# Optimization experiments

Hardware: AMD Instinct MI355X
Metric: run time of the kernel (lower is better)

The kernel has to match this reference:

```python
import jax, jax.numpy as jnp
import numpy as np

STATE_DIM = 5
HIDDEN = 32
B, S = 128, 4096
D_IN = STATE_DIM + 1 + 3  # [h_prev, temp_seq, direction]


def setup_inputs() -> dict:
    key = jax.random.key(0)
    ks = jax.random.split(key, 16)
    g = lambda k, shp: (jax.random.normal(k, shp, dtype=jnp.float32) * 0.1)
    z = lambda shp: jnp.zeros(shp, jnp.float32)
    inp = {}
    inp["h_prev"] = jax.random.normal(ks[0], (B, S, STATE_DIM), dtype=jnp.float32)
    inp["delta_x"] = jax.random.uniform(ks[1], (B, S, 6), dtype=jnp.float32)
    # internal layer 0 (input D_IN -> HIDDEN), layer 1 (HIDDEN -> HIDDEN)
    inp["Wa0"] = g(ks[2], (D_IN, HIDDEN)); inp["ba0"] = z((HIDDEN,))
    inp["Wb0"] = g(ks[3], (D_IN, HIDDEN)); inp["bb0"] = z((HIDDEN,))
    inp["Wa1"] = g(ks[4], (HIDDEN, HIDDEN)); inp["ba1"] = z((HIDDEN,))
    inp["Wb1"] = g(ks[5], (HIDDEN, HIDDEN)); inp["bb1"] = z((HIDDEN,))
    inp["W_alpha"] = g(ks[6], (HIDDEN, 1)); inp["b_alpha"] = z((1,))
    inp["W_beta"]  = g(ks[7], (HIDDEN, 1)); inp["b_beta"]  = z((1,))
    inp["W_gamma"] = g(ks[8], (HIDDEN, 1)); inp["b_gamma"] = z((1,))
    inp["W_c"] = g(ks[9], (HIDDEN, STATE_DIM)); inp["b_c"] = z((STATE_DIM,))
    inp["W_out"] = g(ks[10], (STATE_DIM, 1))  # no bias
    return inp


def reference(h_prev, delta_x, Wa0, ba0, Wb0, bb0, Wa1, ba1, Wb1, bb1,
              W_alpha, b_alpha, W_beta, b_beta, W_gamma, b_gamma,
              W_c, b_c, W_out):
    # delta_x: [delta_strain, delta_time, delta_temp, init_strain, init_time, init_temp]
    df = delta_x[..., :3]                       # (B, S, 3)
    init_temp = delta_x[:, 0:1, 5:6]            # (B, 1, 1) init temp at t=0
    temp_seq = jnp.cumsum(delta_x[..., 2:3], axis=1) + init_temp  # (B, S, 1)
    # normalized increment direction
    norm = jnp.maximum(jnp.sqrt(jnp.sum(df * df, axis=-1, keepdims=True)), 1e-7)
    direction = df / norm                       # (B, S, 3)
    l = jnp.concatenate([h_prev, temp_seq, direction], axis=-1)   # (B, S, 9)
    # two internal tanh*tanh gated dense layers
    l = jnp.tanh(l @ Wa0 + ba0) * jnp.tanh(l @ Wb0 + bb0)         # (B, S, 32)
    l = jnp.tanh(l @ Wa1 + ba1) * jnp.tanh(l @ Wb1 + bb1)         # (B, S, 32)
    # exp gates (non-negative rate params)
    alpha = jnp.exp(l @ W_alpha + b_alpha)      # (B, S, 1)
    beta  = jnp.exp(l @ W_beta  + b_beta)
    gamma = jnp.exp(l @ W_gamma + b_gamma)
    c_n = jnp.tanh(l @ W_c + b_c)               # (B, S, 5)
    # update gate from physical increments
    z = 1.0 - jnp.exp(-alpha * jnp.abs(df[..., 0:1])
                      - beta * df[..., 1:2]
                      - gamma * jnp.abs(df[..., 2:3]))
    h_n = (1.0 - z) * h_prev + z * c_n          # (B, S, 5)
    sigma_n = h_n @ W_out                       # (B, S, 1)
    return (h_n, sigma_n)
```

## Files before the change

kernel.cpp:

```cpp
#include <hip/hip_runtime.h>

#define B_DIMC   128
#define S_DIMC   4096
#define N_TOK    (B_DIMC * S_DIMC)
#define CHUNK    256
#define N_CHUNK  (N_TOK / CHUNK)
#define CPB      (S_DIMC / CHUNK)

typedef __attribute__((ext_vector_type(8))) short  short8;
typedef __attribute__((ext_vector_type(4))) float  floatx4;
typedef __attribute__((ext_vector_type(4))) int    intx4;

__device__ float g_chunksums[N_CHUNK];

__device__ __forceinline__ unsigned short f2bf(float f) {
    unsigned u = __builtin_bit_cast(unsigned, f);
    u = (u + 0x7FFFu + ((u >> 16) & 1u)) >> 16;
    return (unsigned short)u;
}
__device__ __forceinline__ int packbf(float a, float b) {
    return (int)f2bf(a) | ((int)f2bf(b) << 16);
}
__device__ __forceinline__ float fast_tanh(float x) {
    float xc = fminf(fmaxf(x, -9.0f), 9.0f);
    float e  = __builtin_amdgcn_exp2f(2.885390082f * xc);
    return fmaf(-2.0f, __builtin_amdgcn_rcpf(e + 1.0f), 1.0f);
}

__global__ __launch_bounds__(256) void chunksum_kernel(const float* __restrict__ dx) {
    const int t    = blockIdx.x * CHUNK + threadIdx.x;
    const int lane = threadIdx.x & 63;
    const int wid  = threadIdx.x >> 6;
    __shared__ float wsum[4];
    float x = dx[(size_t)t * 6 + 2];
    #pragma unroll
    for (int off = 32; off >= 1; off >>= 1) x += __shfl_down(x, off, 64);
    if (lane == 0) wsum[wid] = x;
    __syncthreads();
    if (threadIdx.x == 0)
        g_chunksums[blockIdx.x] = wsum[0] + wsum[1] + wsum[2] + wsum[3];
}

__device__ __forceinline__ float head_w(int n, int k,
                                        const float* Wal, const float* Wbe,
                                        const float* Wga, const float* Wc) {
    if (n == 0) return Wal[k];
    if (n == 1) return Wbe[k];
    if (n == 2) return Wga[k];
    if (n < 8)  return Wc[k * 5 + (n - 3)];
    return 0.0f;
}

__global__ __launch_bounds__(256) void msc_kernel(
    const float* __restrict__ h_prev, const float* __restrict__ dx,
    const float* __restrict__ Wa0, const float* __restrict__ ba0,
    const float* __restrict__ Wb0, const float* __restrict__ bb0,
    const float* __restrict__ Wa1, const float* __restrict__ ba1,
    const float* __restrict__ Wb1, const float* __restrict__ bb1,
    const float* __restrict__ W_alpha, const float* __restrict__ b_alpha,
    const float* __restrict__ W_beta,  const float* __restrict__ b_beta,
    const float* __restrict__ W_gamma, const float* __restrict__ b_gamma,
    const float* __restrict__ W_c,     const float* __restrict__ b_c,
    const float* __restrict__ W_out,
    float* __restrict__ out)
{
    __shared__ __align__(16) short sW[4][32][40];
    __shared__ __align__(16) short sWh[16][40];
    __shared__ __align__(16) short sA[4][64][40];
    __shared__ __align__(16) float sTemps[4][64];
    __shared__ float sBias[16];
    __shared__ float sWsum[4];

    const int tid  = threadIdx.x;
    const int w    = tid >> 6;
    const int lane = tid & 63;
    const int n    = lane & 15;
    const int quad = lane >> 4;
    const int t    = blockIdx.x * CHUNK + tid;

    const float* hp = h_prev + (size_t)t * 5;
    const float* d  = dx     + (size_t)t * 6;
    const float hp0 = hp[0], hp1 = hp[1], hp2 = hp[2], hp3 = hp[3], hp4 = hp[4];
    const float df0 = d[0], df1 = d[1], df2 = d[2];

    const int batch = blockIdx.x / CPB;
    const int cib   = blockIdx.x % CPB;
    float coff = dx[(size_t)batch * S_DIMC * 6 + 5];
    #pragma unroll
    for (int c = 0; c < CPB - 1; ++c)
        if (c < cib) coff += g_chunksums[batch * CPB + c];

    float w5a[2], w5b[2], bA0[2], bB0[2], bA1[2], bB1[2];
    #pragma unroll
    for (int nt = 0; nt < 2; ++nt) {
        const int col = nt * 16 + n;
        w5a[nt] = Wa0[5 * 32 + col];  w5b[nt] = Wb0[5 * 32 + col];
        bA0[nt] = ba0[col];           bB0[nt] = bb0[col];
        bA1[nt] = ba1[col];           bB1[nt] = bb1[col];
    }

    float x = df2;
    #pragma unroll
    for (int off = 1; off < 64; off <<= 1) {
        float y = __shfl_up(x, off, 64);
        if (lane >= off) x += y;
    }
    if (lane == 63) sWsum[w] = x;

    const float nrm = fmaxf(sqrtf(df0*df0 + df1*df1 + df2*df2), 1e-7f);
    const float inv = __builtin_amdgcn_rcpf(nrm);
    {
        int* arow = (int*)&sA[w][lane][0];
        intx4 v0 = { packbf(hp0, hp1), packbf(hp2, hp3),
                     packbf(hp4, 0.0f), packbf(df0*inv, df1*inv) };
        intx4 v1 = { packbf(df2*inv, 0.0f), 0, 0, 0 };
        intx4 z  = { 0, 0, 0, 0 };
        *(intx4*)&arow[0]  = v0;
        *(intx4*)&arow[4]  = v1;
        *(intx4*)&arow[8]  = z;
        *(intx4*)&arow[12] = z;
    }

    #pragma unroll
    for (int m = 0; m < 4; ++m) {
        const float* Wsrc = (m == 0) ? Wa0 : (m == 1) ? Wb0 : (m == 2) ? Wa1 : Wb1;
        const bool l0 = (m < 2);
        #pragma unroll
        for (int dd = tid; dd < 512; dd += 256) {
            const int col = dd >> 4, kd = dd & 15, k0 = kd * 2, k1 = k0 + 1;
            float v0, v1;
            if (l0) {
                v0 = (k0 < 9 && k0 != 5) ? Wsrc[k0 * 32 + col] : 0.0f;
                v1 = (k1 < 9 && k1 != 5) ? Wsrc[k1 * 32 + col] : 0.0f;
            } else {
                v0 = Wsrc[k0 * 32 + col];
                v1 = Wsrc[k1 * 32 + col];
            }
            ((int*)&sW[m][col][0])[kd] = packbf(v0, v1);
        }
    }
    {
        const int hn = tid >> 4, kd = tid & 15, k0 = kd * 2;
        const float v0 = head_w(hn, k0,     W_alpha, W_beta, W_gamma, W_c);
        const float v1 = head_w(hn, k0 + 1, W_alpha, W_beta, W_gamma, W_c);
        ((int*)&sWh[hn][0])[kd] = packbf(v0, v1);
    }
    if (tid < 16) {
        sBias[tid] = (tid == 0) ? b_alpha[0] : (tid == 1) ? b_beta[0]
                   : (tid == 2) ? b_gamma[0] : (tid < 8) ? b_c[tid - 3] : 0.0f;
    }

    __syncthreads();

    float pre = coff;
    if (w > 0) pre += sWsum[0];
    if (w > 1) pre += sWsum[1];
    if (w > 2) pre += sWsum[2];
    const float temp_t = pre + x;
    sTemps[w][lane] = temp_t;

    short8 Ba0f[2], Bb0f[2], Ba1f[2], Bb1f[2], Bhf;
    #pragma unroll
    for (int nt = 0; nt < 2; ++nt) {
        const int col = nt * 16 + n;
        Ba0f[nt] = *(const short8*)&sW[0][col][quad * 8];
        Bb0f[nt] = *(const short8*)&sW[1][col][quad * 8];
        Ba1f[nt] = *(const short8*)&sW[2][col][quad * 8];
        Bb1f[nt] = *(const short8*)&sW[3][col][quad * 8];
    }
    Bhf = *(const short8*)&sWh[n][quad * 8];
    const float hbias = sBias[n];

    #pragma unroll
    for (int mt = 0; mt < 4; ++mt) {
        const short8  Af = *(const short8*)&sA[w][mt * 16 + n][quad * 8];
        const floatx4 tv = *(const floatx4*)&sTemps[w][mt * 16 + quad * 4];
        #pragma unroll
        for (int nt = 0; nt < 2; ++nt) {
            floatx4 Ca, Cb;
            #pragma unroll
            for (int r = 0; r < 4; ++r) {
                Ca[r] = fmaf(tv[r], w5a[nt], bA0[nt]);
                Cb[r] = fmaf(tv[r], w5b[nt], bB0[nt]);
            }
            Ca = __builtin_amdgcn_mfma_f32_16x16x32_bf16(Af, Ba0f[nt], Ca, 0, 0, 0);
            Cb = __builtin_amdgcn_mfma_f32_16x16x32_bf16(Af, Bb0f[nt], Cb, 0, 0, 0);
            #pragma unroll
            for (int r = 0; r < 4; ++r) {
                const float gv = fast_tanh(Ca[r]) * fast_tanh(Cb[r]);
                sA[w][mt * 16 + quad * 4 + r][nt * 16 + n] = (short)f2bf(gv);
            }
        }
    }

    #pragma unroll
    for (int mt = 0; mt < 4; ++mt) {
        const short8 Af = *(const short8*)&sA[w][mt * 16 + n][quad * 8];
        #pragma unroll
        for (int nt = 0; nt < 2; ++nt) {
            floatx4 Ca = { bA1[nt], bA1[nt], bA1[nt], bA1[nt] };
            floatx4 Cb = { bB1[nt], bB1[nt], bB1[nt], bB1[nt] };
            Ca = __builtin_amdgcn_mfma_f32_16x16x32_bf16(Af, Ba1f[nt], Ca, 0, 0, 0);
            Cb = __builtin_amdgcn_mfma_f32_16x16x32_bf16(Af, Bb1f[nt], Cb, 0, 0, 0);
            #pragma unroll
            for (int r = 0; r < 4; ++r) {
                const float gv = fast_tanh(Ca[r]) * fast_tanh(Cb[r]);
                sA[w][mt * 16 + quad * 4 + r][nt * 16 + n] = (short)f2bf(gv);
            }
        }
    }

    short8 Ah[4];
    #pragma unroll
    for (int mt = 0; mt < 4; ++mt)
        Ah[mt] = *(const short8*)&sA[w][mt * 16 + n][quad * 8];
    __syncthreads();

    float* hc = (float*)&sA[w][0][0];
    #pragma unroll
    for (int mt = 0; mt < 4; ++mt) {
        floatx4 C = { hbias, hbias, hbias, hbias };
        C = __builtin_amdgcn_mfma_f32_16x16x32_bf16(Ah[mt], Bhf, C, 0, 0, 0);
        if (n < 8) {
            #pragma unroll
            for (int r = 0; r < 4; ++r)
                hc[(mt * 16 + quad * 4 + r) * 12 + n] = C[r];
        }
    }

    const floatx4 h0v = *(const floatx4*)&hc[lane * 12];
    const floatx4 h1v = *(const floatx4*)&hc[lane * 12 + 4];

    const float alpha = __expf(h0v[0]);
    const float beta  = __expf(h0v[1]);
    const float gamma = __expf(h0v[2]);
    const float z     = 1.0f - __expf(-(alpha * fabsf(df0) + beta * df1 + gamma * fabsf(df2)));
    const float omz   = 1.0f - z;

    const float c0 = fast_tanh(h0v[3]), c1 = fast_tanh(h1v[0]), c2 = fast_tanh(h1v[1]),
                c3 = fast_tanh(h1v[2]), c4 = fast_tanh(h1v[3]);

    const float hn0 = omz * hp0 + z * c0;
    const float hn1 = omz * hp1 + z * c1;
    const float hn2 = omz * hp2 + z * c2;
    const float hn3 = omz * hp3 + z * c3;
    const float hn4 = omz * hp4 + z * c4;

    float* out_h = out + (size_t)t * 5;
    out_h[0] = hn0; out_h[1] = hn1; out_h[2] = hn2; out_h[3] = hn3; out_h[4] = hn4;
    out[(size_t)N_TOK * 5 + t] =
        hn0 * W_out[0] + hn1 * W_out[1] + hn2 * W_out[2] + hn3 * W_out[3] + hn4 * W_out[4];
}

extern "C" void kernel_launch(void* const* d_in, const int* in_sizes, int n_in,
                              void* d_out, int out_size, void* d_ws, size_t ws_size,
                              hipStream_t stream) {
    const float* h_prev  = (const float*)d_in[0];
    const float* dx      = (const float*)d_in[1];
    const float* Wa0     = (const float*)d_in[2];
    const float* ba0     = (const float*)d_in[3];
    const float* Wb0     = (const float*)d_in[4];
    const float* bb0     = (const float*)d_in[5];
    const float* Wa1     = (const float*)d_in[6];
    const float* ba1     = (const float*)d_in[7];
    const float* Wb1     = (const float*)d_in[8];
    const float* bb1     = (const float*)d_in[9];
    const float* W_alpha = (const float*)d_in[10];
    const float* b_alpha = (const float*)d_in[11];
    const float* W_beta  = (const float*)d_in[12];
    const float* b_beta  = (const float*)d_in[13];
    const float* W_gamma = (const float*)d_in[14];
    const float* b_gamma = (const float*)d_in[15];
    const float* W_c     = (const float*)d_in[16];
    const float* b_c     = (const float*)d_in[17];
    const float* W_out   = (const float*)d_in[18];
    float* out = (float*)d_out;

    chunksum_kernel<<<N_CHUNK, CHUNK, 0, stream>>>(dx);
    msc_kernel<<<N_CHUNK, CHUNK, 0, stream>>>(
        h_prev, dx,
        Wa0, ba0, Wb0, bb0, Wa1, ba1, Wb1, bb1,
        W_alpha, b_alpha, W_beta, b_beta, W_gamma, b_gamma,
        W_c, b_c, W_out, out);
}
```

Measured before the change: 137.3 us.

## Load MFMA weight fragments directly to registers and fuse tanh-gate product

Weight B-fragments are now built per lane straight from global memory into registers, removing the shared-memory weight staging and its bias array. The chunk-prefix offset becomes a lane-parallel xor-shuffle reduction instead of a serial loop. The tanh*tanh gate is merged algebraically into one reciprocal and uses fmed3 clamping, and launch bounds request 7 blocks per CU. This cuts LDS footprint and per-element transcendental work, but each lane now issues more scattered global loads of weights and needs more registers.

```diff
diff --git a/kernel.cpp b/kernel.cpp
--- a/kernel.cpp
+++ b/kernel.cpp
@@ -22,9 +22,16 @@
     return (int)f2bf(a) | ((int)f2bf(b) << 16);
 }
 __device__ __forceinline__ float fast_tanh(float x) {
-    float xc = fminf(fmaxf(x, -9.0f), 9.0f);
-    float e  = __builtin_amdgcn_exp2f(2.885390082f * xc);
+    float e = __builtin_amdgcn_exp2f(2.885390082f * __builtin_amdgcn_fmed3f(x, -9.0f, 9.0f));
     return fmaf(-2.0f, __builtin_amdgcn_rcpf(e + 1.0f), 1.0f);
+}
+__device__ __forceinline__ float gate2(float a, float b) {
+    const float c = 2.885390082f;
+    float ea = __builtin_amdgcn_exp2f(c * __builtin_amdgcn_fmed3f(a, -9.0f, 9.0f));
+    float eb = __builtin_amdgcn_exp2f(c * __builtin_amdgcn_fmed3f(b, -9.0f, 9.0f));
+    float t  = fmaf(ea, eb, 1.0f);
+    float u  = ea + eb;
+    return (t - u) * __builtin_amdgcn_rcpf(t + u);
 }
 
 __global__ __launch_bounds__(256) void chunksum_kernel(const float* __restrict__ dx) {
@@ -41,17 +48,52 @@
         g_chunksums[blockIdx.x] = wsum[0] + wsum[1] + wsum[2] + wsum[3];
 }
 
-__device__ __forceinline__ float head_w(int n, int k,
-                                        const float* Wal, const float* Wbe,
-                                        const float* Wga, const float* Wc) {
-    if (n == 0) return Wal[k];
-    if (n == 1) return Wbe[k];
-    if (n == 2) return Wga[k];
-    if (n < 8)  return Wc[k * 5 + (n - 3)];
-    return 0.0f;
-}
-
-__global__ __launch_bounds__(256) void msc_kernel(
+__device__ __forceinline__ short8 zero8() {
+    short8 z = { 0, 0, 0, 0, 0, 0, 0, 0 };
+    return z;
+}
+__device__ __forceinline__ short8 load_bfrag_l0(const float* __restrict__ W, int col, int quad) {
+    short8 f = zero8();
+    if (quad == 0) {
+        float v[8];
+        #pragma unroll
+        for (int j = 0; j < 8; ++j) v[j] = (j == 5) ? 0.0f : W[j * 32 + col];
+        #pragma unroll
+        for (int jp = 0; jp < 4; ++jp) ((int*)&f)[jp] = packbf(v[2*jp], v[2*jp+1]);
+    } else if (quad == 1) {
+        ((int*)&f)[0] = packbf(W[8 * 32 + col], 0.0f);
+    }
+    return f;
+}
+__device__ __forceinline__ short8 load_bfrag(const float* __restrict__ W, int col, int quad) {
+    short8 f;
+    #pragma unroll
+    for (int jp = 0; jp < 4; ++jp) {
+        const int k = quad * 8 + jp * 2;
+        ((int*)&f)[jp] = packbf(W[k * 32 + col], W[(k + 1) * 32 + col]);
+    }
+    return f;
+}
+__device__ __forceinline__ short8 load_bfrag_head(int n, int quad,
+        const float* __restrict__ Wal, const float* __restrict__ Wbe,
+        const float* __restrict__ Wga, const float* __restrict__ Wc) {
+    short8 f = zero8();
+    if (n < 8) {
+        #pragma unroll
+        for (int jp = 0; jp < 4; ++jp) {
+            const int k0 = quad * 8 + jp * 2, k1 = k0 + 1;
+            float v0, v1;
+            if      (n == 0) { v0 = Wal[k0]; v1 = Wal[k1]; }
+            else if (n == 1) { v0 = Wbe[k0]; v1 = Wbe[k1]; }
+            else if (n == 2) { v0 = Wga[k0]; v1 = Wga[k1]; }
+            else             { v0 = Wc[k0 * 5 + (n - 3)]; v1 = Wc[k1 * 5 + (n - 3)]; }
+            ((int*)&f)[jp] = packbf(v0, v1);
+        }
+    }
+    return f;
+}
+
+__global__ __launch_bounds__(256, 7) void msc_kernel(
     const float* __restrict__ h_prev, const float* __restrict__ dx,
     const float* __restrict__ Wa0, const float* __restrict__ ba0,
     const float* __restrict__ Wb0, const float* __restrict__ bb0,
@@ -64,11 +106,8 @@
     const float* __restrict__ W_out,
     float* __restrict__ out)
 {
-    __shared__ __align__(16) short sW[4][32][40];
-    __shared__ __align__(16) short sWh[16][40];
     __shared__ __align__(16) short sA[4][64][40];
     __shared__ __align__(16) float sTemps[4][64];
-    __shared__ float sBias[16];
     __shared__ float sWsum[4];
 
     const int tid  = threadIdx.x;
@@ -85,10 +124,10 @@
 
     const int batch = blockIdx.x / CPB;
     const int cib   = blockIdx.x % CPB;
-    float coff = dx[(size_t)batch * S_DIMC * 6 + 5];
-    #pragma unroll
-    for (int c = 0; c < CPB - 1; ++c)
-        if (c < cib) coff += g_chunksums[batch * CPB + c];
+    float cs = (lane < cib) ? g_chunksums[batch * CPB + lane] : 0.0f;
+    #pragma unroll
+    for (int m = 1; m < 64; m <<= 1) cs += __shfl_xor(cs, m, 64);
+    const float coff = dx[(size_t)batch * S_DIMC * 6 + 5] + cs;
 
     float w5a[2], w5b[2], bA0[2], bB0[2], bA1[2], bB1[2];
     #pragma unroll
@@ -121,34 +160,18 @@
         *(intx4*)&arow[12] = z;
     }
 
-    #pragma unroll
-    for (int m = 0; m < 4; ++m) {
-        const float* Wsrc = (m == 0) ? Wa0 : (m == 1) ? Wb0 : (m == 2) ? Wa1 : Wb1;
-        const bool l0 = (m < 2);
-        #pragma unroll
-        for (int dd = tid; dd < 512; dd += 256) {
-            const int col = dd >> 4, kd = dd & 15, k0 = kd * 2, k1 = k0 + 1;
-            float v0, v1;
-            if (l0) {
-                v0 = (k0 < 9 && k0 != 5) ? Wsrc[k0 * 32 + col] : 0.0f;
-                v1 = (k1 < 9 && k1 != 5) ? Wsrc[k1 * 32 + col] : 0.0f;
-            } else {
-                v0 = Wsrc[k0 * 32 + col];
-                v1 = Wsrc[k1 * 32 + col];
-            }
-            ((int*)&sW[m][col][0])[kd] = packbf(v0, v1);
-        }
-    }
-    {
-        const int hn = tid >> 4, kd = tid & 15, k0 = kd * 2;
-        const float v0 = head_w(hn, k0,     W_alpha, W_beta, W_gamma, W_c);
-        const float v1 = head_w(hn, k0 + 1, W_alpha, W_beta, W_gamma, W_c);
-        ((int*)&sWh[hn][0])[kd] = packbf(v0, v1);
-    }
-    if (tid < 16) {
-        sBias[tid] = (tid == 0) ? b_alpha[0] : (tid == 1) ? b_beta[0]
-                   : (tid == 2) ? b_gamma[0] : (tid < 8) ? b_c[tid - 3] : 0.0f;
-    }
+    short8 Ba0f[2], Bb0f[2], Ba1f[2], Bb1f[2], Bhf;
+    #pragma unroll
+    for (int nt = 0; nt < 2; ++nt) {
+        const int col = nt * 16 + n;
+        Ba0f[nt] = load_bfrag_l0(Wa0, col, quad);
+        Bb0f[nt] = load_bfrag_l0(Wb0, col, quad);
+        Ba1f[nt] = load_bfrag(Wa1, col, quad);
+        Bb1f[nt] = load_bfrag(Wb1, col, quad);
+    }
+    Bhf = load_bfrag_head(n, quad, W_alpha, W_beta, W_gamma, W_c);
+    const float hbias = (n == 0) ? b_alpha[0] : (n == 1) ? b_beta[0]
+                      : (n == 2) ? b_gamma[0] : (n < 8) ? b_c[n - 3] : 0.0f;
 
     __syncthreads();
 
@@ -159,18 +182,6 @@
     const float temp_t = pre + x;
     sTemps[w][lane] = temp_t;
 
-    short8 Ba0f[2], Bb0f[2], Ba1f[2], Bb1f[2], Bhf;
-    #pragma unroll
-    for (int nt = 0; nt < 2; ++nt) {
-        const int col = nt * 16 + n;
-        Ba0f[nt] = *(const short8*)&sW[0][col][quad * 8];
-        Bb0f[nt] = *(const short8*)&sW[1][col][quad * 8];
-        Ba1f[nt] = *(const short8*)&sW[2][col][quad * 8];
-        Bb1f[nt] = *(const short8*)&sW[3][col][quad * 8];
-    }
-    Bhf = *(const short8*)&sWh[n][quad * 8];
-    const float hbias = sBias[n];
-
     #pragma unroll
     for (int mt = 0; mt < 4; ++mt) {
         const short8  Af = *(const short8*)&sA[w][mt * 16 + n][quad * 8];
@@ -186,10 +197,8 @@
             Ca = __builtin_amdgcn_mfma_f32_16x16x32_bf16(Af, Ba0f[nt], Ca, 0, 0, 0);
             Cb = __builtin_amdgcn_mfma_f32_16x16x32_bf16(Af, Bb0f[nt], Cb, 0, 0, 0);
             #pragma unroll
-            for (int r = 0; r < 4; ++r) {
-                const float gv = fast_tanh(Ca[r]) * fast_tanh(Cb[r]);
-                sA[w][mt * 16 + quad * 4 + r][nt * 16 + n] = (short)f2bf(gv);
-            }
+            for (int r = 0; r < 4; ++r)
+                sA[w][mt * 16 + quad * 4 + r][nt * 16 + n] = (short)f2bf(gate2(Ca[r], Cb[r]));
         }
     }
 
@@ -203,10 +212,8 @@
             Ca = __builtin_amdgcn_mfma_f32_16x16x32_bf16(Af, Ba1f[nt], Ca, 0, 0, 0);
             Cb = __builtin_amdgcn_mfma_f32_16x16x32_bf16(Af, Bb1f[nt], Cb, 0, 0, 0);
             #pragma unroll
-            for (int r = 0; r < 4; ++r) {
-                const float gv = fast_tanh(Ca[r]) * fast_tanh(Cb[r]);
-                sA[w][mt * 16 + quad * 4 + r][nt * 16 + n] = (short)f2bf(gv);
-            }
+            for (int r = 0; r < 4; ++r)
+                sA[w][mt * 16 + quad * 4 + r][nt * 16 + n] = (short)f2bf(gate2(Ca[r], Cb[r]));
         }
     }
 
```

After: 161.1 us. +17.3%, slower.

## Alias weight and activation LDS, fuse tanh product, parallelize chunk offset sum

Applied to the files above, without the earlier changes.

Puts the weight staging buffers and the activation tile in one shared-memory union, so the kernel uses less LDS and more blocks can be resident. This needs an extra barrier before the activation tile overwrites the weights. The gated product tanh(a)*tanh(b) is computed with a single reciprocal through an algebraic identity, and the clamp uses fmed3. The prefix of chunk sums is now computed with a wave-wide xor reduction instead of a serial loop.

```diff
diff --git a/kernel.cpp b/kernel.cpp
--- a/kernel.cpp
+++ b/kernel.cpp
@@ -22,9 +22,16 @@
     return (int)f2bf(a) | ((int)f2bf(b) << 16);
 }
 __device__ __forceinline__ float fast_tanh(float x) {
-    float xc = fminf(fmaxf(x, -9.0f), 9.0f);
-    float e  = __builtin_amdgcn_exp2f(2.885390082f * xc);
+    float e = __builtin_amdgcn_exp2f(2.885390082f * __builtin_amdgcn_fmed3f(x, -9.0f, 9.0f));
     return fmaf(-2.0f, __builtin_amdgcn_rcpf(e + 1.0f), 1.0f);
+}
+__device__ __forceinline__ float gate2(float a, float b) {
+    const float c = 2.885390082f;
+    float ea = __builtin_amdgcn_exp2f(c * __builtin_amdgcn_fmed3f(a, -9.0f, 9.0f));
+    float eb = __builtin_amdgcn_exp2f(c * __builtin_amdgcn_fmed3f(b, -9.0f, 9.0f));
+    float t  = fmaf(ea, eb, 1.0f);
+    float u  = ea + eb;
+    return (t - u) * __builtin_amdgcn_rcpf(t + u);
 }
 
 __global__ __launch_bounds__(256) void chunksum_kernel(const float* __restrict__ dx) {
@@ -50,6 +57,15 @@
     if (n < 8)  return Wc[k * 5 + (n - 3)];
     return 0.0f;
 }
+
+union SMemU {
+    struct {
+        short W[4][32][40];
+        short Wh[16][40];
+        float Bias[16];
+    } b;
+    short A[4][64][40];
+};
 
 __global__ __launch_bounds__(256) void msc_kernel(
     const float* __restrict__ h_prev, const float* __restrict__ dx,
@@ -64,11 +80,8 @@
     const float* __restrict__ W_out,
     float* __restrict__ out)
 {
-    __shared__ __align__(16) short sW[4][32][40];
-    __shared__ __align__(16) short sWh[16][40];
-    __shared__ __align__(16) short sA[4][64][40];
+    __shared__ __align__(16) SMemU sm;
     __shared__ __align__(16) float sTemps[4][64];
-    __shared__ float sBias[16];
     __shared__ float sWsum[4];
 
     const int tid  = threadIdx.x;
@@ -85,10 +98,10 @@
 
     const int batch = blockIdx.x / CPB;
     const int cib   = blockIdx.x % CPB;
-    float coff = dx[(size_t)batch * S_DIMC * 6 + 5];
-    #pragma unroll
-    for (int c = 0; c < CPB - 1; ++c)
-        if (c < cib) coff += g_chunksums[batch * CPB + c];
+    float cs = (lane < cib) ? g_chunksums[batch * CPB + lane] : 0.0f;
+    #pragma unroll
+    for (int m = 1; m < 64; m <<= 1) cs += __shfl_xor(cs, m, 64);
+    const float coff = dx[(size_t)batch * S_DIMC * 6 + 5] + cs;
 
     float w5a[2], w5b[2], bA0[2], bB0[2], bA1[2], bB1[2];
     #pragma unroll
@@ -106,20 +119,6 @@
         if (lane >= off) x += y;
     }
     if (lane == 63) sWsum[w] = x;
-
-    const float nrm = fmaxf(sqrtf(df0*df0 + df1*df1 + df2*df2), 1e-7f);
-    const float inv = __builtin_amdgcn_rcpf(nrm);
-    {
-        int* arow = (int*)&sA[w][lane][0];
-        intx4 v0 = { packbf(hp0, hp1), packbf(hp2, hp3),
-                     packbf(hp4, 0.0f), packbf(df0*inv, df1*inv) };
-        intx4 v1 = { packbf(df2*inv, 0.0f), 0, 0, 0 };
-        intx4 z  = { 0, 0, 0, 0 };
-        *(intx4*)&arow[0]  = v0;
-        *(intx4*)&arow[4]  = v1;
-        *(intx4*)&arow[8]  = z;
-        *(intx4*)&arow[12] = z;
-    }
 
     #pragma unroll
     for (int m = 0; m < 4; ++m) {
@@ -136,44 +135,61 @@
                 v0 = Wsrc[k0 * 32 + col];
                 v1 = Wsrc[k1 * 32 + col];
             }
-            ((int*)&sW[m][col][0])[kd] = packbf(v0, v1);
+            ((int*)&sm.b.W[m][col][0])[kd] = packbf(v0, v1);
         }
     }
     {
         const int hn = tid >> 4, kd = tid & 15, k0 = kd * 2;
         const float v0 = head_w(hn, k0,     W_alpha, W_beta, W_gamma, W_c);
         const float v1 = head_w(hn, k0 + 1, W_alpha, W_beta, W_gamma, W_c);
-        ((int*)&sWh[hn][0])[kd] = packbf(v0, v1);
+        ((int*)&sm.b.Wh[hn][0])[kd] = packbf(v0, v1);
     }
     if (tid < 16) {
-        sBias[tid] = (tid == 0) ? b_alpha[0] : (tid == 1) ? b_beta[0]
-                   : (tid == 2) ? b_gamma[0] : (tid < 8) ? b_c[tid - 3] : 0.0f;
-    }
-
-    __syncthreads();
+        sm.b.Bias[tid] = (tid == 0) ? b_alpha[0] : (tid == 1) ? b_beta[0]
+                       : (tid == 2) ? b_gamma[0] : (tid < 8) ? b_c[tid - 3] : 0.0f;
+    }
+
+    __syncthreads();
+
+    short8 Ba0f[2], Bb0f[2], Ba1f[2], Bb1f[2], Bhf;
+    #pragma unroll
+    for (int nt = 0; nt < 2; ++nt) {
+        const int col = nt * 16 + n;
+        Ba0f[nt] = *(const short8*)&sm.b.W[0][col][quad * 8];
+        Bb0f[nt] = *(const short8*)&sm.b.W[1][col][quad * 8];
+        Ba1f[nt] = *(const short8*)&sm.b.W[2][col][quad * 8];
+        Bb1f[nt] = *(const short8*)&sm.b.W[3][col][quad * 8];
+    }
+    Bhf = *(const short8*)&sm.b.Wh[n][quad * 8];
+    const float hbias = sm.b.Bias[n];
 
     float pre = coff;
     if (w > 0) pre += sWsum[0];
     if (w > 1) pre += sWsum[1];
     if (w > 2) pre += sWsum[2];
     const float temp_t = pre + x;
+
+    __syncthreads();
+
     sTemps[w][lane] = temp_t;
 
-    short8 Ba0f[2], Bb0f[2], Ba1f[2], Bb1f[2], Bhf;
-    #pragma unroll
-    for (int nt = 0; nt < 2; ++nt) {
-        const int col = nt * 16 + n;
-        Ba0f[nt] = *(const short8*)&sW[0][col][quad * 8];
-        Bb0f[nt] = *(const short8*)&sW[1][col][quad * 8];
-        Ba1f[nt] = *(const short8*)&sW[2][col][quad * 8];
-        Bb1f[nt] = *(const short8*)&sW[3][col][quad * 8];
-    }
-    Bhf = *(const short8*)&sWh[n][quad * 8];
-    const float hbias = sBias[n];
+    const float nrm = fmaxf(sqrtf(df0*df0 + df1*df1 + df2*df2), 1e-7f);
+    const float inv = __builtin_amdgcn_rcpf(nrm);
+    {
+        int* arow = (int*)&sm.A[w][lane][0];
+        intx4 v0 = { packbf(hp0, hp1), packbf(hp2, hp3),
+                     packbf(hp4, 0.0f), packbf(df0*inv, df1*inv) };
+        intx4 v1 = { packbf(df2*inv, 0.0f), 0, 0, 0 };
+        intx4 z  = { 0, 0, 0, 0 };
+        *(intx4*)&arow[0]  = v0;
+        *(intx4*)&arow[4]  = v1;
+        *(intx4*)&arow[8]  = z;
+        *(intx4*)&arow[12] = z;
+    }
 
     #pragma unroll
     for (int mt = 0; mt < 4; ++mt) {
-        const short8  Af = *(const short8*)&sA[w][mt * 16 + n][quad * 8];
+        const short8  Af = *(const short8*)&sm.A[w][mt * 16 + n][quad * 8];
         const floatx4 tv = *(const floatx4*)&sTemps[w][mt * 16 + quad * 4];
         #pragma unroll
         for (int nt = 0; nt < 2; ++nt) {
@@ -186,16 +202,14 @@
             Ca = __builtin_amdgcn_mfma_f32_16x16x32_bf16(Af, Ba0f[nt], Ca, 0, 0, 0);
             Cb = __builtin_amdgcn_mfma_f32_16x16x32_bf16(Af, Bb0f[nt], Cb, 0, 0, 0);
             #pragma unroll
-            for (int r = 0; r < 4; ++r) {
-                const float gv = fast_tanh(Ca[r]) * fast_tanh(Cb[r]);
-                sA[w][mt * 16 + quad * 4 + r][nt * 16 + n] = (short)f2bf(gv);
-            }
+            for (int r = 0; r < 4; ++r)
+                sm.A[w][mt * 16 + quad * 4 + r][nt * 16 + n] = (short)f2bf(gate2(Ca[r], Cb[r]));
         }
     }
 
     #pragma unroll
     for (int mt = 0; mt < 4; ++mt) {
-        const short8 Af = *(const short8*)&sA[w][mt * 16 + n][quad * 8];
+        const short8 Af = *(const short8*)&sm.A[w][mt * 16 + n][quad * 8];
         #pragma unroll
         for (int nt = 0; nt < 2; ++nt) {
             floatx4 Ca = { bA1[nt], bA1[nt], bA1[nt], bA1[nt] };
@@ -203,20 +217,18 @@
             Ca = __builtin_amdgcn_mfma_f32_16x16x32_bf16(Af, Ba1f[nt], Ca, 0, 0, 0);
             Cb = __builtin_amdgcn_mfma_f32_16x16x32_bf16(Af, Bb1f[nt], Cb, 0, 0, 0);
             #pragma unroll
-            for (int r = 0; r < 4; ++r) {
-                const float gv = fast_tanh(Ca[r]) * fast_tanh(Cb[r]);
-                sA[w][mt * 16 + quad * 4 + r][nt * 16 + n] = (short)f2bf(gv);
-            }
+            for (int r = 0; r < 4; ++r)
+                sm.A[w][mt * 16 + quad * 4 + r][nt * 16 + n] = (short)f2bf(gate2(Ca[r], Cb[r]));
         }
     }
 
     short8 Ah[4];
     #pragma unroll
     for (int mt = 0; mt < 4; ++mt)
-        Ah[mt] = *(const short8*)&sA[w][mt * 16 + n][quad * 8];
-    __syncthreads();
-
-    float* hc = (float*)&sA[w][0][0];
+        Ah[mt] = *(const short8*)&sm.A[w][mt * 16 + n][quad * 8];
+    __syncthreads();
+
+    float* hc = (float*)&sm.A[w][0][0];
     #pragma unroll
     for (int mt = 0; mt < 4; ++mt) {
         floatx4 C = { hbias, hbias, hbias, hbias };
```

Result: faster. 132.9 us (-3.3%).
